# Optimization experiments

Measured on AMD Instinct MI355X. Metric: run time of the kernel, lower is better.

Reference implementation:

```python
import jax, jax.numpy as jnp
import numpy as np

N = 100000
E = 3200000
F_IN = 128
H1, C1 = 2, 16          # conv1: heads=2, out_channels=16, concat -> 32
H2, C2 = 1, 40          # conv2: heads=1, out_channels=num_classes=40
NEG_SLOPE = 0.2


def setup_inputs() -> dict:
    key = jax.random.key(0)
    ks = jax.random.split(key, 12)
    features = jax.random.normal(ks[0], (N, F_IN), dtype=jnp.float32)
    edges = jax.random.randint(ks[1], (2, E), 0, N, dtype=jnp.int64)
    weight = jax.random.uniform(ks[2], (E,), dtype=jnp.float32)  # ignored (edge_dim=None)
    s = 0.1
    W1 = jax.random.normal(ks[3], (F_IN, H1 * C1), dtype=jnp.float32) * s
    att_src1 = jax.random.normal(ks[4], (H1, C1), dtype=jnp.float32) * s
    att_dst1 = jax.random.normal(ks[5], (H1, C1), dtype=jnp.float32) * s
    b1 = jnp.zeros((H1 * C1,), dtype=jnp.float32)
    W2 = jax.random.normal(ks[6], (H1 * C1, H2 * C2), dtype=jnp.float32) * s
    att_src2 = jax.random.normal(ks[7], (H2, C2), dtype=jnp.float32) * s
    att_dst2 = jax.random.normal(ks[8], (H2, C2), dtype=jnp.float32) * s
    b2 = jnp.zeros((H2 * C2,), dtype=jnp.float32)
    return {"features": features, "edges": edges, "weight": weight,
            "W1": W1, "att_src1": att_src1, "att_dst1": att_dst1, "b1": b1,
            "W2": W2, "att_src2": att_src2, "att_dst2": att_dst2, "b2": b2}


def _segment_softmax(e, seg, num_segments):
    # e: [E, H]; softmax over edges sharing the same destination node
    m = jax.ops.segment_max(e, seg, num_segments=num_segments)
    ex = jnp.exp(e - m[seg])
    s = jax.ops.segment_sum(ex, seg, num_segments=num_segments)
    return ex / (s[seg] + 1e-16)


def _gat_conv(x, src, dst, W, att_src, att_dst, bias, heads, out_ch):
    n = x.shape[0]
    h = (x @ W).reshape(n, heads, out_ch)                  # [N,H,C]
    a_src = jnp.sum(h * att_src, axis=-1)                  # [N,H]
    a_dst = jnp.sum(h * att_dst, axis=-1)                  # [N,H]
    e = a_src[src] + a_dst[dst]                            # [E,H]
    e = jnp.where(e > 0, e, NEG_SLOPE * e)                 # LeakyReLU(0.2)
    alpha = _segment_softmax(e, dst, n)                    # [E,H]
    msg = h[src] * alpha[:, :, None]                       # [E,H,C]
    out = jax.ops.segment_sum(msg, dst, num_segments=n)    # [N,H,C]
    return out.reshape(n, heads * out_ch) + bias           # concat=True


def reference(features, edges, weight, W1, att_src1, att_dst1, b1,
              W2, att_src2, att_dst2, b2):
    n = features.shape[0]
    # GATConv default add_self_loops=True (self-loop removal of pre-existing
    # loops skipped: negligible for random edges and not jit-shape-friendly)
    loop = jnp.arange(n, dtype=edges.dtype)
    src = jnp.concatenate([edges[0], loop])
    dst = jnp.concatenate([edges[1], loop])
    x = _gat_conv(features, src, dst, W1, att_src1, att_dst1, b1, H1, C1)
    x = jax.nn.relu(x)
    # F.dropout with training=self.training -> identity in eval mode
    x = _gat_conv(x, src, dst, W2, att_src2, att_dst2, b2, H2, C2)
    return x
```

## Files before the change

### kernel.cpp

```cpp
#include <hip/hip_runtime.h>


#define DEVFN __device__ __forceinline__
#define CB_SHIFT 9
#define CB_SZ 512
#define CHUNK 8192
#define A2B 250

DEVFN unsigned short f2h(float f) {
  _Float16 h = (_Float16)f;
  unsigned short u;
  __builtin_memcpy(&u, &h, 2);
  return u;
}
DEVFN float h2f(unsigned short u) {
  _Float16 h;
  __builtin_memcpy(&h, &u, 2);
  return (float)h;
}

__global__ void detect_kernel(const int* eg32, int E, int* flag) {
  __shared__ int any;
  if (threadIdx.x == 0) any = 0;
  __syncthreads();
  for (int k = threadIdx.x; k < 2048 && k < E; k += 256) {
    if (eg32[2 * k + 1] != 0) atomicOr(&any, 1);
  }
  __syncthreads();
  if (threadIdx.x == 0) flag[0] = any ? 0 : 1;
}

DEVFN int read_dst(const long long* eg64, const int* eg32, int is64, int E, int i) {
  if (i >= E) return i - E;
  return is64 ? (int)eg64[E + i] : eg32[E + i];
}

DEVFN void read_edge(const long long* eg64, const int* eg32, int is64, int E,
                     int i, int& s, int& d) {
  if (i >= E) { s = d = i - E; return; }
  if (is64) { s = (int)eg64[i]; d = (int)eg64[E + i]; }
  else      { s = eg32[i];      d = eg32[E + i]; }
}

__global__ void scan_blocks(const int* __restrict__ cnt, int* __restrict__ rp,
                            int* __restrict__ bsum, int n) {
  __shared__ int buf[2][1024];
  int t = threadIdx.x;
  int gid = blockIdx.x * 1024 + t;
  int v = (gid < n) ? cnt[gid] : 0;
  buf[0][t] = v;
  __syncthreads();
  int pin = 0;
  for (int offd = 1; offd < 1024; offd <<= 1) {
    int nv = buf[pin][t];
    if (t >= offd) nv += buf[pin][t - offd];
    buf[1 - pin][t] = nv;
    pin = 1 - pin;
    __syncthreads();
  }
  int inc = buf[pin][t];
  if (gid < n) rp[gid] = inc - v;
  if (t == 1023) bsum[blockIdx.x] = inc;
}

__global__ void scan_sums(const int* bsum, int* boff, int nb) {
  if (blockIdx.x == 0 && threadIdx.x == 0) {
    int r = 0;
    for (int i = 0; i < nb; i++) { boff[i] = r; r += bsum[i]; }
  }
}

__global__ void scan_add(int* rp, const int* boff, int n, int total) {
  int i = blockIdx.x * 1024 + threadIdx.x;
  if (i < n) rp[i] = rp[i] + boff[blockIdx.x];
  if (i == 0) rp[n] = total;
}

__global__ __launch_bounds__(256) void chunk_hist(const long long* eg64,
                                                  const int* eg32, const int* flag,
                                                  int E, int N, int NWG,
                                                  int* __restrict__ histg) {
  __shared__ int lh[CB_SZ];
  int w = blockIdx.x, t = threadIdx.x;
  int NB2 = (N + CB_SZ - 1) / CB_SZ;
  for (int j = t; j < NB2; j += 256) lh[j] = 0;
  __syncthreads();
  int is64 = flag[0];
  int EN = E + N;
  int i0 = w * CHUNK;
  int i1 = i0 + CHUNK; if (i1 > EN) i1 = EN;
  for (int i = i0 + t; i < i1; i += 256) {
    int d = read_dst(eg64, eg32, is64, E, i);
    atomicAdd(&lh[d >> CB_SHIFT], 1);
  }
  __syncthreads();
  for (int b = t; b < NB2; b += 256) histg[b * NWG + w] = lh[b];
}

__global__ __launch_bounds__(256) void chunk_scatter(const long long* eg64,
                                                     const int* eg32, const int* flag,
                                                     int E, int N, int NWG,
                                                     const int* __restrict__ hists,
                                                     int* __restrict__ tmp) {
  __shared__ int lcur[CB_SZ];
  int w = blockIdx.x, t = threadIdx.x;
  int NB2 = (N + CB_SZ - 1) / CB_SZ;
  for (int b = t; b < NB2; b += 256) lcur[b] = hists[b * NWG + w];
  __syncthreads();
  int is64 = flag[0];
  int EN = E + N;
  int i0 = w * CHUNK;
  int i1 = i0 + CHUNK; if (i1 > EN) i1 = EN;
  for (int i = i0 + t; i < i1; i += 256) {
    int s, d;
    read_edge(eg64, eg32, is64, E, i, s, d);
    int b = d >> CB_SHIFT;
    int pos = atomicAdd(&lcur[b], 1);
    tmp[pos] = (s << CB_SHIFT) | (d & (CB_SZ - 1));
  }
}

__global__ __launch_bounds__(256) void bucket_rp_sort(const int* __restrict__ hists,
                                                      int NWG,
                                                      const int* __restrict__ tmp,
                                                      int* __restrict__ rp,
                                                      int* __restrict__ csr,
                                                      int N, int EN) {
  __shared__ int lc[CB_SZ];
  __shared__ int ps[256];
  __shared__ int lcur[CB_SZ];
  int b = blockIdx.x, t = threadIdx.x;
  for (int j = t; j < CB_SZ; j += 256) lc[j] = 0;
  __syncthreads();
  int w0 = hists[b * NWG];
  int w1 = hists[(b + 1) * NWG];
  for (int p = w0 + t; p < w1; p += 256)
    atomicAdd(&lc[tmp[p] & (CB_SZ - 1)], 1);
  __syncthreads();
  int a = lc[2 * t], c = lc[2 * t + 1];
  ps[t] = a + c;
  __syncthreads();
  for (int off = 1; off < 256; off <<= 1) {
    int v = ps[t];
    int u = (t >= off) ? ps[t - off] : 0;
    __syncthreads();
    ps[t] = v + u;
    __syncthreads();
  }
  int base = w0 + ps[t] - (a + c);
  lcur[2 * t] = base;
  lcur[2 * t + 1] = base + a;
  int n0 = b * CB_SZ;
  if (n0 + 2 * t < N) rp[n0 + 2 * t] = base;
  if (n0 + 2 * t + 1 < N) rp[n0 + 2 * t + 1] = base + a;
  if (b == (int)gridDim.x - 1 && t == 0) rp[N] = EN;
  __syncthreads();
  for (int p = w0 + t; p < w1; p += 256) {
    int e = tmp[p];
    int dl = e & (CB_SZ - 1);
    int s = e >> CB_SHIFT;
    int pos = atomicAdd(&lcur[dl], 1);
    csr[pos] = s;
  }
}

__global__ __launch_bounds__(256) void gemm1f(const float* __restrict__ X,
                                              const float* __restrict__ W,
                                              const float* __restrict__ att_s,
                                              const float* __restrict__ att_d,
                                              uint4* __restrict__ h1h,
                                              float* __restrict__ as1,
                                              float* __restrict__ ad1, int N) {
  __shared__ float Wl[128 * 32];
  __shared__ float Asl[32], Adl[32];
  int t = threadIdx.x;
  for (int i = t; i < 1024; i += 256)
    ((float4*)Wl)[i] = ((const float4*)W)[i];
  if (t < 32) { Asl[t] = att_s[t]; Adl[t] = att_d[t]; }
  __syncthreads();
  int n = blockIdx.x * 256 + t;
  if (n >= N) return;
  const float4* X4 = (const float4*)(X + (size_t)n * 128);
  float acc[32];
#pragma unroll
  for (int c = 0; c < 32; c++) acc[c] = 0.f;
  for (int k4 = 0; k4 < 32; k4++) {
    float4 x = X4[k4];
    const float4* w4 = (const float4*)(Wl + k4 * 128);
#pragma unroll
    for (int c4 = 0; c4 < 8; c4++) {
      float4 w0 = w4[c4], w1 = w4[8 + c4], w2 = w4[16 + c4], w3 = w4[24 + c4];
      float* A = acc + c4 * 4;
      A[0] = fmaf(x.x, w0.x, A[0]); A[1] = fmaf(x.x, w0.y, A[1]);
      A[2] = fmaf(x.x, w0.z, A[2]); A[3] = fmaf(x.x, w0.w, A[3]);
      A[0] = fmaf(x.y, w1.x, A[0]); A[1] = fmaf(x.y, w1.y, A[1]);
      A[2] = fmaf(x.y, w1.z, A[2]); A[3] = fmaf(x.y, w1.w, A[3]);
      A[0] = fmaf(x.z, w2.x, A[0]); A[1] = fmaf(x.z, w2.y, A[1]);
      A[2] = fmaf(x.z, w2.z, A[2]); A[3] = fmaf(x.z, w2.w, A[3]);
      A[0] = fmaf(x.w, w3.x, A[0]); A[1] = fmaf(x.w, w3.y, A[1]);
      A[2] = fmaf(x.w, w3.z, A[2]); A[3] = fmaf(x.w, w3.w, A[3]);
    }
  }
  float s0 = 0.f, d0 = 0.f, s1 = 0.f, d1 = 0.f;
#pragma unroll
  for (int c = 0; c < 16; c++) {
    s0 = fmaf(acc[c], Asl[c], s0);
    d0 = fmaf(acc[c], Adl[c], d0);
    s1 = fmaf(acc[16 + c], Asl[16 + c], s1);
    d1 = fmaf(acc[16 + c], Adl[16 + c], d1);
  }
  as1[n * 2] = s0; as1[n * 2 + 1] = s1;
  ad1[n * 2] = d0; ad1[n * 2 + 1] = d1;
#pragma unroll
  for (int j = 0; j < 4; j++) {
    uint4 u;
    u.x = (unsigned)f2h(acc[j * 8 + 0]) | ((unsigned)f2h(acc[j * 8 + 1]) << 16);
    u.y = (unsigned)f2h(acc[j * 8 + 2]) | ((unsigned)f2h(acc[j * 8 + 3]) << 16);
    u.z = (unsigned)f2h(acc[j * 8 + 4]) | ((unsigned)f2h(acc[j * 8 + 5]) << 16);
    u.w = (unsigned)f2h(acc[j * 8 + 6]) | ((unsigned)f2h(acc[j * 8 + 7]) << 16);
    h1h[(size_t)n * 4 + j] = u;
  }
}

__global__ __launch_bounds__(256) void gemm2f(const float* __restrict__ X,
                                              const float* __restrict__ W,
                                              const float* __restrict__ att_s,
                                              const float* __restrict__ att_d,
                                              uint4* __restrict__ h2h,
                                              float* __restrict__ as2,
                                              float* __restrict__ ad2, int N) {
  __shared__ float Wl[32 * 40];
  __shared__ float Asl[40], Adl[40];
  int t = threadIdx.x;
  for (int i = t; i < 320; i += 256)
    ((float4*)Wl)[i] = ((const float4*)W)[i];
  if (t < 40) { Asl[t] = att_s[t]; Adl[t] = att_d[t]; }
  __syncthreads();
  int n = blockIdx.x * 256 + t;
  if (n >= N) return;
  const float4* X4 = (const float4*)(X + (size_t)n * 32);
  float acc[40];
#pragma unroll
  for (int c = 0; c < 40; c++) acc[c] = 0.f;
  for (int k4 = 0; k4 < 8; k4++) {
    float4 x = X4[k4];
    const float4* w4 = (const float4*)(Wl + k4 * 160);
#pragma unroll
    for (int c4 = 0; c4 < 10; c4++) {
      float4 w0 = w4[c4], w1 = w4[10 + c4], w2 = w4[20 + c4], w3 = w4[30 + c4];
      float* A = acc + c4 * 4;
      A[0] = fmaf(x.x, w0.x, A[0]); A[1] = fmaf(x.x, w0.y, A[1]);
      A[2] = fmaf(x.x, w0.z, A[2]); A[3] = fmaf(x.x, w0.w, A[3]);
      A[0] = fmaf(x.y, w1.x, A[0]); A[1] = fmaf(x.y, w1.y, A[1]);
      A[2] = fmaf(x.y, w1.z, A[2]); A[3] = fmaf(x.y, w1.w, A[3]);
      A[0] = fmaf(x.z, w2.x, A[0]); A[1] = fmaf(x.z, w2.y, A[1]);
      A[2] = fmaf(x.z, w2.z, A[2]); A[3] = fmaf(x.z, w2.w, A[3]);
      A[0] = fmaf(x.w, w3.x, A[0]); A[1] = fmaf(x.w, w3.y, A[1]);
      A[2] = fmaf(x.w, w3.z, A[2]); A[3] = fmaf(x.w, w3.w, A[3]);
    }
  }
  float ss = 0.f, sd = 0.f;
#pragma unroll
  for (int c = 0; c < 40; c++) {
    ss = fmaf(acc[c], Asl[c], ss);
    sd = fmaf(acc[c], Adl[c], sd);
  }
  as2[n] = ss; ad2[n] = sd;
#pragma unroll
  for (int j = 0; j < 5; j++) {
    uint4 u;
    u.x = (unsigned)f2h(acc[j * 8 + 0]) | ((unsigned)f2h(acc[j * 8 + 1]) << 16);
    u.y = (unsigned)f2h(acc[j * 8 + 2]) | ((unsigned)f2h(acc[j * 8 + 3]) << 16);
    u.z = (unsigned)f2h(acc[j * 8 + 4]) | ((unsigned)f2h(acc[j * 8 + 5]) << 16);
    u.w = (unsigned)f2h(acc[j * 8 + 6]) | ((unsigned)f2h(acc[j * 8 + 7]) << 16);
    h2h[(size_t)n * 8 + j] = u;
  }
}

__global__ __launch_bounds__(256) void agg1_fused(const int* __restrict__ rp,
                                                  const int* __restrict__ csr,
                                                  const float* __restrict__ as,
                                                  const float* __restrict__ ad,
                                                  const uint4* __restrict__ h1h,
                                                  const float* __restrict__ bias,
                                                  float* __restrict__ x1, int N) {
  int idx = blockIdx.x * 256 + threadIdx.x;
  if (idx >= N * 8) return;
  int n = idx >> 3;
  int half = (idx >> 2) & 1;
  int cq = idx & 3;
  int h = cq >> 1;
  int p0 = rp[n], p1 = rp[n + 1];
  float adv = ad[n * 2 + h];
  float acc[8] = {0, 0, 0, 0, 0, 0, 0, 0};
  float ssum = 0.f;
  int p = p0 + half;
  for (; p + 2 < p1; p += 4) {
    int s0 = csr[p], s1 = csr[p + 2];
    float e0 = as[s0 * 2 + h] + adv;
    float e1 = as[s1 * 2 + h] + adv;
    uint4 u0 = h1h[(size_t)s0 * 4 + cq];
    uint4 u1 = h1h[(size_t)s1 * 4 + cq];
    e0 = e0 > 0.f ? e0 : 0.2f * e0;
    e1 = e1 > 0.f ? e1 : 0.2f * e1;
    float x0 = __expf(e0), x1e = __expf(e1);
    ssum += x0 + x1e;
    acc[0] = fmaf(x0, h2f(u0.x & 0xffff), acc[0]);
    acc[1] = fmaf(x0, h2f(u0.x >> 16),    acc[1]);
    acc[2] = fmaf(x0, h2f(u0.y & 0xffff), acc[2]);
    acc[3] = fmaf(x0, h2f(u0.y >> 16),    acc[3]);
    acc[4] = fmaf(x0, h2f(u0.z & 0xffff), acc[4]);
    acc[5] = fmaf(x0, h2f(u0.z >> 16),    acc[5]);
    acc[6] = fmaf(x0, h2f(u0.w & 0xffff), acc[6]);
    acc[7] = fmaf(x0, h2f(u0.w >> 16),    acc[7]);
    acc[0] = fmaf(x1e, h2f(u1.x & 0xffff), acc[0]);
    acc[1] = fmaf(x1e, h2f(u1.x >> 16),    acc[1]);
    acc[2] = fmaf(x1e, h2f(u1.y & 0xffff), acc[2]);
    acc[3] = fmaf(x1e, h2f(u1.y >> 16),    acc[3]);
    acc[4] = fmaf(x1e, h2f(u1.z & 0xffff), acc[4]);
    acc[5] = fmaf(x1e, h2f(u1.z >> 16),    acc[5]);
    acc[6] = fmaf(x1e, h2f(u1.w & 0xffff), acc[6]);
    acc[7] = fmaf(x1e, h2f(u1.w >> 16),    acc[7]);
  }
  for (; p < p1; p += 2) {
    int s = csr[p];
    float e = as[s * 2 + h] + adv;
    uint4 u = h1h[(size_t)s * 4 + cq];
    e = e > 0.f ? e : 0.2f * e;
    float ex = __expf(e);
    ssum += ex;
    acc[0] = fmaf(ex, h2f(u.x & 0xffff), acc[0]);
    acc[1] = fmaf(ex, h2f(u.x >> 16),    acc[1]);
    acc[2] = fmaf(ex, h2f(u.y & 0xffff), acc[2]);
    acc[3] = fmaf(ex, h2f(u.y >> 16),    acc[3]);
    acc[4] = fmaf(ex, h2f(u.z & 0xffff), acc[4]);
    acc[5] = fmaf(ex, h2f(u.z >> 16),    acc[5]);
    acc[6] = fmaf(ex, h2f(u.w & 0xffff), acc[6]);
    acc[7] = fmaf(ex, h2f(u.w >> 16),    acc[7]);
  }
#pragma unroll
  for (int j = 0; j < 8; j++) acc[j] += __shfl_xor(acc[j], 4);
  ssum += __shfl_xor(ssum, 4);
  float inv = 1.0f / (ssum + 1e-16f);
  float4 bv = ((const float4*)bias)[cq * 2 + half];
  const float* A = acc + half * 4;
  float4 r;
  r.x = fmaxf(fmaf(A[0], inv, bv.x), 0.f);
  r.y = fmaxf(fmaf(A[1], inv, bv.y), 0.f);
  r.z = fmaxf(fmaf(A[2], inv, bv.z), 0.f);
  r.w = fmaxf(fmaf(A[3], inv, bv.w), 0.f);
  ((float4*)x1)[(size_t)n * 8 + cq * 2 + half] = r;
}

__global__ __launch_bounds__(256) void agg2_fused(const int* __restrict__ rp,
                                                  const int* __restrict__ csr,
                                                  const float* __restrict__ as,
                                                  const float* __restrict__ ad,
                                                  const uint4* __restrict__ h2h,
                                                  const float* __restrict__ bias,
                                                  float* __restrict__ outp, int N) {
  __shared__ float part[256][9];
  int t = threadIdx.x;
  int idx = blockIdx.x * A2B + t;
  bool act = (t < A2B) && (idx < N * 10);
  int n = 0, half = 0, cq = 0, p0 = 0, p1 = 0;
  float adv = 0.f;
  if (act) {
    n = idx / 10;
    int r = idx % 10;
    half = r >= 5;
    cq = r - half * 5;
    p0 = rp[n]; p1 = rp[n + 1];
    adv = ad[n];
  }
  float acc[8] = {0, 0, 0, 0, 0, 0, 0, 0};
  float ssum = 0.f;
  if (act) {
    int p = p0 + half;
    for (; p + 2 < p1; p += 4) {
      int s0 = csr[p], s1 = csr[p + 2];
      float e0 = as[s0] + adv;
      float e1 = as[s1] + adv;
      uint4 u0 = h2h[(size_t)s0 * 8 + cq];
      uint4 u1 = h2h[(size_t)s1 * 8 + cq];
      e0 = e0 > 0.f ? e0 : 0.2f * e0;
      e1 = e1 > 0.f ? e1 : 0.2f * e1;
      float x0 = __expf(e0), x1e = __expf(e1);
      ssum += x0 + x1e;
      acc[0] = fmaf(x0, h2f(u0.x & 0xffff), acc[0]);
      acc[1] = fmaf(x0, h2f(u0.x >> 16),    acc[1]);
      acc[2] = fmaf(x0, h2f(u0.y & 0xffff), acc[2]);
      acc[3] = fmaf(x0, h2f(u0.y >> 16),    acc[3]);
      acc[4] = fmaf(x0, h2f(u0.z & 0xffff), acc[4]);
      acc[5] = fmaf(x0, h2f(u0.z >> 16),    acc[5]);
      acc[6] = fmaf(x0, h2f(u0.w & 0xffff), acc[6]);
      acc[7] = fmaf(x0, h2f(u0.w >> 16),    acc[7]);
      acc[0] = fmaf(x1e, h2f(u1.x & 0xffff), acc[0]);
      acc[1] = fmaf(x1e, h2f(u1.x >> 16),    acc[1]);
      acc[2] = fmaf(x1e, h2f(u1.y & 0xffff), acc[2]);
      acc[3] = fmaf(x1e, h2f(u1.y >> 16),    acc[3]);
      acc[4] = fmaf(x1e, h2f(u1.z & 0xffff), acc[4]);
      acc[5] = fmaf(x1e, h2f(u1.z >> 16),    acc[5]);
      acc[6] = fmaf(x1e, h2f(u1.w & 0xffff), acc[6]);
      acc[7] = fmaf(x1e, h2f(u1.w >> 16),    acc[7]);
    }
    for (; p < p1; p += 2) {
      int s = csr[p];
      float e = as[s] + adv;
      uint4 u = h2h[(size_t)s * 8 + cq];
      e = e > 0.f ? e : 0.2f * e;
      float ex = __expf(e);
      ssum += ex;
      acc[0] = fmaf(ex, h2f(u.x & 0xffff), acc[0]);
      acc[1] = fmaf(ex, h2f(u.x >> 16),    acc[1]);
      acc[2] = fmaf(ex, h2f(u.y & 0xffff), acc[2]);
      acc[3] = fmaf(ex, h2f(u.y >> 16),    acc[3]);
      acc[4] = fmaf(ex, h2f(u.z & 0xffff), acc[4]);
      acc[5] = fmaf(ex, h2f(u.z >> 16),    acc[5]);
      acc[6] = fmaf(ex, h2f(u.w & 0xffff), acc[6]);
      acc[7] = fmaf(ex, h2f(u.w >> 16),    acc[7]);
    }
  }
  if (act && half) {
#pragma unroll
    for (int j = 0; j < 8; j++) part[t][j] = acc[j];
    part[t][8] = ssum;
  }
  __syncthreads();
  if (act && !half) {
#pragma unroll
    for (int j = 0; j < 8; j++) acc[j] += part[t + 5][j];
    ssum += part[t + 5][8];
    float inv = 1.0f / (ssum + 1e-16f);
    const float4* b4 = (const float4*)bias;
    float4 ba = b4[cq * 2], bb = b4[cq * 2 + 1];
    float4 r0, r1;
    r0.x = fmaf(acc[0], inv, ba.x);
    r0.y = fmaf(acc[1], inv, ba.y);
    r0.z = fmaf(acc[2], inv, ba.z);
    r0.w = fmaf(acc[3], inv, ba.w);
    r1.x = fmaf(acc[4], inv, bb.x);
    r1.y = fmaf(acc[5], inv, bb.y);
    r1.z = fmaf(acc[6], inv, bb.z);
    r1.w = fmaf(acc[7], inv, bb.w);
    ((float4*)outp)[(size_t)n * 10 + cq * 2]     = r0;
    ((float4*)outp)[(size_t)n * 10 + cq * 2 + 1] = r1;
  }
}

extern "C" void kernel_launch(void* const* d_in, const int* in_sizes, int n_in,
                              void* d_out, int out_size, void* d_ws, size_t ws_size,
                              hipStream_t stream) {
  const float* X    = (const float*)d_in[0];
  const long long* eg64 = (const long long*)d_in[1];
  const int* eg32   = (const int*)d_in[1];
  const float* W1   = (const float*)d_in[3];
  const float* as1w = (const float*)d_in[4];
  const float* ad1w = (const float*)d_in[5];
  const float* b1   = (const float*)d_in[6];
  const float* W2   = (const float*)d_in[7];
  const float* as2w = (const float*)d_in[8];
  const float* ad2w = (const float*)d_in[9];
  const float* b2   = (const float*)d_in[10];
  float* out = (float*)d_out;

  const int N  = in_sizes[0] / 128;
  const int E  = in_sizes[1] / 2;
  const int EN = E + N;
  const int NB2 = (N + CB_SZ - 1) / CB_SZ;
  const int NWG = (EN + CHUNK - 1) / CHUNK;
  const int NH  = NB2 * NWG;

  char* wbase = (char*)d_ws;
  size_t off = 0;
  auto alloc = [&](size_t bytes) -> void* {
    void* p = wbase + off;
    off += (bytes + 255) & ~(size_t)255;
    return p;
  };

  uint4* h1h = (uint4*)alloc((size_t)N * 64);
  uint4* h2h = (uint4*)alloc((size_t)N * 128);
  float* x1  = (float*)alloc((size_t)N * 32 * 4);
  float* as1 = (float*)alloc((size_t)N * 2 * 4);
  float* ad1 = (float*)alloc((size_t)N * 2 * 4);
  float* as2 = (float*)alloc((size_t)N * 4);
  float* ad2 = (float*)alloc((size_t)N * 4);
  int* rp     = (int*)alloc((size_t)(N + 1) * 4);
  int* histg  = (int*)alloc((size_t)NH * 4);
  int* hists  = (int*)alloc((size_t)(NH + 1) * 4);
  int* bsum   = (int*)alloc(1024 * 4);
  int* boff   = (int*)alloc(1024 * 4);
  int* flag   = (int*)alloc(256);
  int* csr    = (int*)alloc((size_t)EN * 4);
  int* tmp    = (int*)alloc((size_t)EN * 4);
  (void)ws_size; (void)n_in; (void)out_size;

  const int gN  = (N + 255) / 256;
  const int nbH = (NH + 1023) / 1024;

  detect_kernel<<<1, 256, 0, stream>>>(eg32, E, flag);

  chunk_hist<<<NWG, 256, 0, stream>>>(eg64, eg32, flag, E, N, NWG, histg);
  scan_blocks<<<nbH, 1024, 0, stream>>>(histg, hists, bsum, NH);
  scan_sums<<<1, 64, 0, stream>>>(bsum, boff, nbH);
  scan_add<<<nbH, 1024, 0, stream>>>(hists, boff, NH, EN);
  chunk_scatter<<<NWG, 256, 0, stream>>>(eg64, eg32, flag, E, N, NWG, hists, tmp);
  bucket_rp_sort<<<NB2, 256, 0, stream>>>(hists, NWG, tmp, rp, csr, N, EN);

  gemm1f<<<gN, 256, 0, stream>>>(X, W1, as1w, ad1w, h1h, as1, ad1, N);
  agg1_fused<<<(N * 8 + 255) / 256, 256, 0, stream>>>(rp, csr, as1, ad1, h1h, b1, x1, N);

  gemm2f<<<gN, 256, 0, stream>>>(x1, W2, as2w, ad2w, h2h, as2, ad2, N);
  agg2_fused<<<(N * 10 + A2B - 1) / A2B, 256, 0, stream>>>(rp, csr, as2, ad2, h2h, b2, out, N);
}
```

Measured before the change: 392.3 us.

## Fuse layer-1 aggregation with layer-2 GEMM and inline int64 detection

Merges agg1 and gemm2 into one kernel that keeps the 32-wide hidden row in shared memory and computes the 40-wide projection plus attention scores, removing the x1 global write and re-read and one launch. It also drops the separate detect kernel by doing a per-block ballot check inside the sort kernels. The bucket size and chunk size for CSR construction are halved, which changes the block counts and shared-memory footprint of the sort stages. The fused kernel does more shared-memory traffic and adds barriers inside an aggregation that is bound by irregular gathers.

```diff
diff --git a/kernel.cpp b/kernel.cpp
--- a/kernel.cpp
+++ b/kernel.cpp
@@ -2,9 +2,9 @@
 
 
 #define DEVFN __device__ __forceinline__
-#define CB_SHIFT 9
-#define CB_SZ 512
-#define CHUNK 8192
+#define CB_SHIFT 8
+#define CB_SZ 256
+#define CHUNK 4096
 #define A2B 250
 
 DEVFN unsigned short f2h(float f) {
@@ -19,27 +19,20 @@
   return (float)h;
 }
 
-__global__ void detect_kernel(const int* eg32, int E, int* flag) {
-  __shared__ int any;
-  if (threadIdx.x == 0) any = 0;
-  __syncthreads();
-  for (int k = threadIdx.x; k < 2048 && k < E; k += 256) {
-    if (eg32[2 * k + 1] != 0) atomicOr(&any, 1);
-  }
-  __syncthreads();
-  if (threadIdx.x == 0) flag[0] = any ? 0 : 1;
-}
-
-DEVFN int read_dst(const long long* eg64, const int* eg32, int is64, int E, int i) {
-  if (i >= E) return i - E;
-  return is64 ? (int)eg64[E + i] : eg32[E + i];
-}
-
 DEVFN void read_edge(const long long* eg64, const int* eg32, int is64, int E,
                      int i, int& s, int& d) {
   if (i >= E) { s = d = i - E; return; }
   if (is64) { s = (int)eg64[i]; d = (int)eg64[E + i]; }
   else      { s = eg32[i];      d = eg32[E + i]; }
+}
+
+DEVFN int detect64(const int* eg32, int E, int i0, int t) {
+  int base = i0;
+  if (base > E - 64) base = E - 64;
+  if (base < 0) base = 0;
+  int i = base + (t & 63);
+  unsigned long long m = __ballot((i < E) && (eg32[2 * i + 1] != 0));
+  return m == 0ull;
 }
 
 __global__ void scan_blocks(const int* __restrict__ cnt, int* __restrict__ rp,
@@ -77,20 +70,22 @@
 }
 
 __global__ __launch_bounds__(256) void chunk_hist(const long long* eg64,
-                                                  const int* eg32, const int* flag,
+                                                  const int* eg32,
                                                   int E, int N, int NWG,
                                                   int* __restrict__ histg) {
-  __shared__ int lh[CB_SZ];
+  __shared__ int lh[512];
   int w = blockIdx.x, t = threadIdx.x;
   int NB2 = (N + CB_SZ - 1) / CB_SZ;
   for (int j = t; j < NB2; j += 256) lh[j] = 0;
-  __syncthreads();
-  int is64 = flag[0];
+  int i0 = w * CHUNK;
+  int is64 = detect64(eg32, E, i0, t);
+  __syncthreads();
   int EN = E + N;
-  int i0 = w * CHUNK;
   int i1 = i0 + CHUNK; if (i1 > EN) i1 = EN;
   for (int i = i0 + t; i < i1; i += 256) {
-    int d = read_dst(eg64, eg32, is64, E, i);
+    int d;
+    if (i >= E) d = i - E;
+    else d = is64 ? (int)eg64[E + i] : eg32[E + i];
     atomicAdd(&lh[d >> CB_SHIFT], 1);
   }
   __syncthreads();
@@ -98,18 +93,18 @@
 }
 
 __global__ __launch_bounds__(256) void chunk_scatter(const long long* eg64,
-                                                     const int* eg32, const int* flag,
+                                                     const int* eg32,
                                                      int E, int N, int NWG,
                                                      const int* __restrict__ hists,
                                                      int* __restrict__ tmp) {
-  __shared__ int lcur[CB_SZ];
+  __shared__ int lcur[512];
   int w = blockIdx.x, t = threadIdx.x;
   int NB2 = (N + CB_SZ - 1) / CB_SZ;
   for (int b = t; b < NB2; b += 256) lcur[b] = hists[b * NWG + w];
-  __syncthreads();
-  int is64 = flag[0];
+  int i0 = w * CHUNK;
+  int is64 = detect64(eg32, E, i0, t);
+  __syncthreads();
   int EN = E + N;
-  int i0 = w * CHUNK;
   int i1 = i0 + CHUNK; if (i1 > EN) i1 = EN;
   for (int i = i0 + t; i < i1; i += 256) {
     int s, d;
@@ -126,19 +121,19 @@
                                                       int* __restrict__ rp,
                                                       int* __restrict__ csr,
                                                       int N, int EN) {
-  __shared__ int lc[CB_SZ];
+  __shared__ int lc[256];
   __shared__ int ps[256];
-  __shared__ int lcur[CB_SZ];
+  __shared__ int lcur[256];
   int b = blockIdx.x, t = threadIdx.x;
-  for (int j = t; j < CB_SZ; j += 256) lc[j] = 0;
+  lc[t] = 0;
   __syncthreads();
   int w0 = hists[b * NWG];
   int w1 = hists[(b + 1) * NWG];
   for (int p = w0 + t; p < w1; p += 256)
     atomicAdd(&lc[tmp[p] & (CB_SZ - 1)], 1);
   __syncthreads();
-  int a = lc[2 * t], c = lc[2 * t + 1];
-  ps[t] = a + c;
+  int my = lc[t];
+  ps[t] = my;
   __syncthreads();
   for (int off = 1; off < 256; off <<= 1) {
     int v = ps[t];
@@ -147,20 +142,16 @@
     ps[t] = v + u;
     __syncthreads();
   }
-  int base = w0 + ps[t] - (a + c);
-  lcur[2 * t] = base;
-  lcur[2 * t + 1] = base + a;
-  int n0 = b * CB_SZ;
-  if (n0 + 2 * t < N) rp[n0 + 2 * t] = base;
-  if (n0 + 2 * t + 1 < N) rp[n0 + 2 * t + 1] = base + a;
+  int base = w0 + ps[t] - my;
+  lcur[t] = base;
+  int n0 = b * CB_SZ + t;
+  if (n0 < N) rp[n0] = base;
   if (b == (int)gridDim.x - 1 && t == 0) rp[N] = EN;
   __syncthreads();
   for (int p = w0 + t; p < w1; p += 256) {
     int e = tmp[p];
-    int dl = e & (CB_SZ - 1);
-    int s = e >> CB_SHIFT;
-    int pos = atomicAdd(&lcur[dl], 1);
-    csr[pos] = s;
+    int pos = atomicAdd(&lcur[e & (CB_SZ - 1)], 1);
+    csr[pos] = e >> CB_SHIFT;
   }
 }
 
@@ -222,134 +213,123 @@
   }
 }
 
-__global__ __launch_bounds__(256) void gemm2f(const float* __restrict__ X,
-                                              const float* __restrict__ W,
-                                              const float* __restrict__ att_s,
-                                              const float* __restrict__ att_d,
-                                              uint4* __restrict__ h2h,
-                                              float* __restrict__ as2,
-                                              float* __restrict__ ad2, int N) {
+__global__ __launch_bounds__(256) void agg1_gemm2(
+    const int* __restrict__ rp, const int* __restrict__ csr,
+    const float* __restrict__ as, const float* __restrict__ ad,
+    const uint4* __restrict__ h1h, const float* __restrict__ b1,
+    const float* __restrict__ W2, const float* __restrict__ as2w,
+    const float* __restrict__ ad2w, uint4* __restrict__ h2h,
+    float* __restrict__ as2, float* __restrict__ ad2, int N) {
   __shared__ float Wl[32 * 40];
-  __shared__ float Asl[40], Adl[40];
+  __shared__ float As2l[40], Ad2l[40];
+  __shared__ float x1t[32][33];
+  __shared__ float h2r[32][41];
   int t = threadIdx.x;
   for (int i = t; i < 320; i += 256)
-    ((float4*)Wl)[i] = ((const float4*)W)[i];
-  if (t < 40) { Asl[t] = att_s[t]; Adl[t] = att_d[t]; }
-  __syncthreads();
-  int n = blockIdx.x * 256 + t;
-  if (n >= N) return;
-  const float4* X4 = (const float4*)(X + (size_t)n * 32);
-  float acc[40];
-#pragma unroll
-  for (int c = 0; c < 40; c++) acc[c] = 0.f;
-  for (int k4 = 0; k4 < 8; k4++) {
-    float4 x = X4[k4];
-    const float4* w4 = (const float4*)(Wl + k4 * 160);
-#pragma unroll
-    for (int c4 = 0; c4 < 10; c4++) {
-      float4 w0 = w4[c4], w1 = w4[10 + c4], w2 = w4[20 + c4], w3 = w4[30 + c4];
-      float* A = acc + c4 * 4;
-      A[0] = fmaf(x.x, w0.x, A[0]); A[1] = fmaf(x.x, w0.y, A[1]);
-      A[2] = fmaf(x.x, w0.z, A[2]); A[3] = fmaf(x.x, w0.w, A[3]);
-      A[0] = fmaf(x.y, w1.x, A[0]); A[1] = fmaf(x.y, w1.y, A[1]);
-      A[2] = fmaf(x.y, w1.z, A[2]); A[3] = fmaf(x.y, w1.w, A[3]);
-      A[0] = fmaf(x.z, w2.x, A[0]); A[1] = fmaf(x.z, w2.y, A[1]);
-      A[2] = fmaf(x.z, w2.z, A[2]); A[3] = fmaf(x.z, w2.w, A[3]);
-      A[0] = fmaf(x.w, w3.x, A[0]); A[1] = fmaf(x.w, w3.y, A[1]);
-      A[2] = fmaf(x.w, w3.z, A[2]); A[3] = fmaf(x.w, w3.w, A[3]);
-    }
-  }
-  float ss = 0.f, sd = 0.f;
-#pragma unroll
-  for (int c = 0; c < 40; c++) {
-    ss = fmaf(acc[c], Asl[c], ss);
-    sd = fmaf(acc[c], Adl[c], sd);
-  }
-  as2[n] = ss; ad2[n] = sd;
-#pragma unroll
-  for (int j = 0; j < 5; j++) {
-    uint4 u;
-    u.x = (unsigned)f2h(acc[j * 8 + 0]) | ((unsigned)f2h(acc[j * 8 + 1]) << 16);
-    u.y = (unsigned)f2h(acc[j * 8 + 2]) | ((unsigned)f2h(acc[j * 8 + 3]) << 16);
-    u.z = (unsigned)f2h(acc[j * 8 + 4]) | ((unsigned)f2h(acc[j * 8 + 5]) << 16);
-    u.w = (unsigned)f2h(acc[j * 8 + 6]) | ((unsigned)f2h(acc[j * 8 + 7]) << 16);
-    h2h[(size_t)n * 8 + j] = u;
-  }
-}
-
-__global__ __launch_bounds__(256) void agg1_fused(const int* __restrict__ rp,
-                                                  const int* __restrict__ csr,
-                                                  const float* __restrict__ as,
-                                                  const float* __restrict__ ad,
-                                                  const uint4* __restrict__ h1h,
-                                                  const float* __restrict__ bias,
-                                                  float* __restrict__ x1, int N) {
-  int idx = blockIdx.x * 256 + threadIdx.x;
-  if (idx >= N * 8) return;
-  int n = idx >> 3;
-  int half = (idx >> 2) & 1;
-  int cq = idx & 3;
+    ((float4*)Wl)[i] = ((const float4*)W2)[i];
+  if (t < 40) { As2l[t] = as2w[t]; Ad2l[t] = ad2w[t]; }
+  int nl = t >> 3, r = t & 7;
+  int half = r >> 2, cq = r & 3;
   int h = cq >> 1;
-  int p0 = rp[n], p1 = rp[n + 1];
-  float adv = ad[n * 2 + h];
+  int n = blockIdx.x * 32 + nl;
   float acc[8] = {0, 0, 0, 0, 0, 0, 0, 0};
   float ssum = 0.f;
-  int p = p0 + half;
-  for (; p + 2 < p1; p += 4) {
-    int s0 = csr[p], s1 = csr[p + 2];
-    float e0 = as[s0 * 2 + h] + adv;
-    float e1 = as[s1 * 2 + h] + adv;
-    uint4 u0 = h1h[(size_t)s0 * 4 + cq];
-    uint4 u1 = h1h[(size_t)s1 * 4 + cq];
-    e0 = e0 > 0.f ? e0 : 0.2f * e0;
-    e1 = e1 > 0.f ? e1 : 0.2f * e1;
-    float x0 = __expf(e0), x1e = __expf(e1);
-    ssum += x0 + x1e;
-    acc[0] = fmaf(x0, h2f(u0.x & 0xffff), acc[0]);
-    acc[1] = fmaf(x0, h2f(u0.x >> 16),    acc[1]);
-    acc[2] = fmaf(x0, h2f(u0.y & 0xffff), acc[2]);
-    acc[3] = fmaf(x0, h2f(u0.y >> 16),    acc[3]);
-    acc[4] = fmaf(x0, h2f(u0.z & 0xffff), acc[4]);
-    acc[5] = fmaf(x0, h2f(u0.z >> 16),    acc[5]);
-    acc[6] = fmaf(x0, h2f(u0.w & 0xffff), acc[6]);
-    acc[7] = fmaf(x0, h2f(u0.w >> 16),    acc[7]);
-    acc[0] = fmaf(x1e, h2f(u1.x & 0xffff), acc[0]);
-    acc[1] = fmaf(x1e, h2f(u1.x >> 16),    acc[1]);
-    acc[2] = fmaf(x1e, h2f(u1.y & 0xffff), acc[2]);
-    acc[3] = fmaf(x1e, h2f(u1.y >> 16),    acc[3]);
-    acc[4] = fmaf(x1e, h2f(u1.z & 0xffff), acc[4]);
-    acc[5] = fmaf(x1e, h2f(u1.z >> 16),    acc[5]);
-    acc[6] = fmaf(x1e, h2f(u1.w & 0xffff), acc[6]);
-    acc[7] = fmaf(x1e, h2f(u1.w >> 16),    acc[7]);
-  }
-  for (; p < p1; p += 2) {
-    int s = csr[p];
-    float e = as[s * 2 + h] + adv;
-    uint4 u = h1h[(size_t)s * 4 + cq];
-    e = e > 0.f ? e : 0.2f * e;
-    float ex = __expf(e);
-    ssum += ex;
-    acc[0] = fmaf(ex, h2f(u.x & 0xffff), acc[0]);
-    acc[1] = fmaf(ex, h2f(u.x >> 16),    acc[1]);
-    acc[2] = fmaf(ex, h2f(u.y & 0xffff), acc[2]);
-    acc[3] = fmaf(ex, h2f(u.y >> 16),    acc[3]);
-    acc[4] = fmaf(ex, h2f(u.z & 0xffff), acc[4]);
-    acc[5] = fmaf(ex, h2f(u.z >> 16),    acc[5]);
-    acc[6] = fmaf(ex, h2f(u.w & 0xffff), acc[6]);
-    acc[7] = fmaf(ex, h2f(u.w >> 16),    acc[7]);
+  if (n < N) {
+    int p0 = rp[n], p1 = rp[n + 1];
+    float adv = ad[n * 2 + h];
+    int p = p0 + half;
+    for (; p + 2 < p1; p += 4) {
+      int s0 = csr[p], s1 = csr[p + 2];
+      float e0 = as[s0 * 2 + h] + adv;
+      float e1 = as[s1 * 2 + h] + adv;
+      uint4 u0 = h1h[(size_t)s0 * 4 + cq];
+      uint4 u1 = h1h[(size_t)s1 * 4 + cq];
+      e0 = e0 > 0.f ? e0 : 0.2f * e0;
+      e1 = e1 > 0.f ? e1 : 0.2f * e1;
+      float x0 = __expf(e0), x1e = __expf(e1);
+      ssum += x0 + x1e;
+      acc[0] = fmaf(x0, h2f(u0.x & 0xffff), acc[0]);
+      acc[1] = fmaf(x0, h2f(u0.x >> 16),    acc[1]);
+      acc[2] = fmaf(x0, h2f(u0.y & 0xffff), acc[2]);
+      acc[3] = fmaf(x0, h2f(u0.y >> 16),    acc[3]);
+      acc[4] = fmaf(x0, h2f(u0.z & 0xffff), acc[4]);
+      acc[5] = fmaf(x0, h2f(u0.z >> 16),    acc[5]);
+      acc[6] = fmaf(x0, h2f(u0.w & 0xffff), acc[6]);
+      acc[7] = fmaf(x0, h2f(u0.w >> 16),    acc[7]);
+      acc[0] = fmaf(x1e, h2f(u1.x & 0xffff), acc[0]);
+      acc[1] = fmaf(x1e, h2f(u1.x >> 16),    acc[1]);
+      acc[2] = fmaf(x1e, h2f(u1.y & 0xffff), acc[2]);
+      acc[3] = fmaf(x1e, h2f(u1.y >> 16),    acc[3]);
+      acc[4] = fmaf(x1e, h2f(u1.z & 0xffff), acc[4]);
+      acc[5] = fmaf(x1e, h2f(u1.z >> 16),    acc[5]);
+      acc[6] = fmaf(x1e, h2f(u1.w & 0xffff), acc[6]);
+      acc[7] = fmaf(x1e, h2f(u1.w >> 16),    acc[7]);
+    }
+    for (; p < p1; p += 2) {
+      int s = csr[p];
+      float e = as[s * 2 + h] + adv;
+      uint4 u = h1h[(size_t)s * 4 + cq];
+      e = e > 0.f ? e : 0.2f * e;
+      float ex = __expf(e);
+      ssum += ex;
+      acc[0] = fmaf(ex, h2f(u.x & 0xffff), acc[0]);
+      acc[1] = fmaf(ex, h2f(u.x >> 16),    acc[1]);
+      acc[2] = fmaf(ex, h2f(u.y & 0xffff), acc[2]);
+      acc[3] = fmaf(ex, h2f(u.y >> 16),    acc[3]);
+      acc[4] = fmaf(ex, h2f(u.z & 0xffff), acc[4]);
+      acc[5] = fmaf(ex, h2f(u.z >> 16),    acc[5]);
+      acc[6] = fmaf(ex, h2f(u.w & 0xffff), acc[6]);
+      acc[7] = fmaf(ex, h2f(u.w >> 16),    acc[7]);
+    }
   }
 #pragma unroll
   for (int j = 0; j < 8; j++) acc[j] += __shfl_xor(acc[j], 4);
   ssum += __shfl_xor(ssum, 4);
-  float inv = 1.0f / (ssum + 1e-16f);
-  float4 bv = ((const float4*)bias)[cq * 2 + half];
-  const float* A = acc + half * 4;
-  float4 r;
-  r.x = fmaxf(fmaf(A[0], inv, bv.x), 0.f);
-  r.y = fmaxf(fmaf(A[1], inv, bv.y), 0.f);
-  r.z = fmaxf(fmaf(A[2], inv, bv.z), 0.f);
-  r.w = fmaxf(fmaf(A[3], inv, bv.w), 0.f);
-  ((float4*)x1)[(size_t)n * 8 + cq * 2 + half] = r;
+  if (n < N) {
+    float inv = 1.0f / (ssum + 1e-16f);
+    float4 bv = ((const float4*)b1)[cq * 2 + half];
+    int ch0 = cq * 8 + half * 4;
+    const float* A = acc + half * 4;
+    x1t[nl][ch0 + 0] = fmaxf(fmaf(A[0], inv, bv.x), 0.f);
+    x1t[nl][ch0 + 1] = fmaxf(fmaf(A[1], inv, bv.y), 0.f);
+    x1t[nl][ch0 + 2] = fmaxf(fmaf(A[2], inv, bv.z), 0.f);
+    x1t[nl][ch0 + 3] = fmaxf(fmaf(A[3], inv, bv.w), 0.f);
+  }
+  __syncthreads();
+  float acc2[5] = {0, 0, 0, 0, 0};
+  int cb = r * 5;
+  if (n < N) {
+    for (int k = 0; k < 32; k++) {
+      float x = x1t[nl][k];
+#pragma unroll
+      for (int c = 0; c < 5; c++)
+        acc2[c] = fmaf(x, Wl[k * 40 + cb + c], acc2[c]);
+    }
+    float ss = 0.f, sd = 0.f;
+#pragma unroll
+    for (int c = 0; c < 5; c++) {
+      ss = fmaf(acc2[c], As2l[cb + c], ss);
+      sd = fmaf(acc2[c], Ad2l[cb + c], sd);
+    }
+#pragma unroll
+    for (int off = 1; off < 8; off <<= 1) {
+      ss += __shfl_xor(ss, off);
+      sd += __shfl_xor(sd, off);
+    }
+    if (r == 0) { as2[n] = ss; ad2[n] = sd; }
+#pragma unroll
+    for (int c = 0; c < 5; c++) h2r[nl][cb + c] = acc2[c];
+  }
+  __syncthreads();
+  if (n < N && r < 5) {
+    const float* hr = h2r[nl] + r * 8;
+    uint4 u;
+    u.x = (unsigned)f2h(hr[0]) | ((unsigned)f2h(hr[1]) << 16);
+    u.y = (unsigned)f2h(hr[2]) | ((unsigned)f2h(hr[3]) << 16);
+    u.z = (unsigned)f2h(hr[4]) | ((unsigned)f2h(hr[5]) << 16);
+    u.w = (unsigned)f2h(hr[6]) | ((unsigned)f2h(hr[7]) << 16);
+    h2h[(size_t)n * 8 + r] = u;
+  }
 }
 
 __global__ __launch_bounds__(256) void agg2_fused(const int* __restrict__ rp,
@@ -481,7 +461,6 @@
 
   uint4* h1h = (uint4*)alloc((size_t)N * 64);
   uint4* h2h = (uint4*)alloc((size_t)N * 128);
-  float* x1  = (float*)alloc((size_t)N * 32 * 4);
   float* as1 = (float*)alloc((size_t)N * 2 * 4);
   float* ad1 = (float*)alloc((size_t)N * 2 * 4);
   float* as2 = (float*)alloc((size_t)N * 4);
@@ -491,7 +470,6 @@
   int* hists  = (int*)alloc((size_t)(NH + 1) * 4);
   int* bsum   = (int*)alloc(1024 * 4);
   int* boff   = (int*)alloc(1024 * 4);
-  int* flag   = (int*)alloc(256);
   int* csr    = (int*)alloc((size_t)EN * 4);
   int* tmp    = (int*)alloc((size_t)EN * 4);
   (void)ws_size; (void)n_in; (void)out_size;
@@ -499,18 +477,16 @@
   const int gN  = (N + 255) / 256;
   const int nbH = (NH + 1023) / 1024;
 
-  detect_kernel<<<1, 256, 0, stream>>>(eg32, E, flag);
-
-  chunk_hist<<<NWG, 256, 0, stream>>>(eg64, eg32, flag, E, N, NWG, histg);
+  chunk_hist<<<NWG, 256, 0, stream>>>(eg64, eg32, E, N, NWG, histg);
   scan_blocks<<<nbH, 1024, 0, stream>>>(histg, hists, bsum, NH);
   scan_sums<<<1, 64, 0, stream>>>(bsum, boff, nbH);
   scan_add<<<nbH, 1024, 0, stream>>>(hists, boff, NH, EN);
-  chunk_scatter<<<NWG, 256, 0, stream>>>(eg64, eg32, flag, E, N, NWG, hists, tmp);
+  chunk_scatter<<<NWG, 256, 0, stream>>>(eg64, eg32, E, N, NWG, hists, tmp);
   bucket_rp_sort<<<NB2, 256, 0, stream>>>(hists, NWG, tmp, rp, csr, N, EN);
 
   gemm1f<<<gN, 256, 0, stream>>>(X, W1, as1w, ad1w, h1h, as1, ad1, N);
-  agg1_fused<<<(N * 8 + 255) / 256, 256, 0, stream>>>(rp, csr, as1, ad1, h1h, b1, x1, N);
-
-  gemm2f<<<gN, 256, 0, stream>>>(x1, W2, as2w, ad2w, h2h, as2, ad2, N);
-  agg2_fused<<<(N * 10 + A2B - 1) / A2B, 256, 0, stream>>>(rp, csr, as2, ad2, h2h, b2, out, N);
-}
+  agg1_gemm2<<<(N + 31) / 32, 256, 0, stream>>>(rp, csr, as1, ad1, h1h, b1,
+                                                W2, as2w, ad2w, h2h, as2, ad2, N);
+  agg2_fused<<<(N * 10 + A2B - 1) / A2B, 256, 0, stream>>>(rp, csr, as2, ad2,
+                                                           h2h, b2, out, N);
+}
```

Result: slower. 406.3 us (+3.6%).
